# Performance work log

Hardware: AMD Instinct MI355X
Metric: run time of the kernel (lower is better)

The kernel has to match this reference:

```python
import jax, jax.numpy as jnp
import numpy as np

NEG_SLOPE = 0.1

def lrelu(x):
    return jnp.where(x >= 0, x, NEG_SLOPE * x)

def conv1d(x, w, b, stride=2):
    # x: [N, C_in, W], w: [C_out, C_in, K], VALID padding, given stride
    y = jax.lax.conv_general_dilated(x, w, (stride,), 'VALID',
                                     dimension_numbers=('NCH', 'OIH', 'NCH'))
    return y + b[None, :, None]

def setup_inputs() -> dict:
    key = jax.random.key(0)
    ks = jax.random.split(key, 16)
    N_NODES = 50000
    N_EDGES = 4950000
    POS_C, CONV_C, CONV_W = 3, 3, 151
    HID, OUT = 256, 1
    W2 = 37  # width after two stride-2 k=3 convs on 151
    IN_G = POS_C + W2  # 40

    def lin_init(k, fan_out, fan_in):
        s = 1.0 / np.sqrt(fan_in)
        k1, k2 = jax.random.split(k)
        return (jax.random.uniform(k1, (fan_out, fan_in), jnp.float32, -s, s),
                jax.random.uniform(k2, (fan_out,), jnp.float32, -s, s))

    pose = jax.random.normal(ks[0], (N_NODES, POS_C), jnp.float32)
    views = jax.random.normal(ks[1], (N_NODES, CONV_C, CONV_W), jnp.float32)
    edge_index = jax.random.randint(ks[2], (2, N_EDGES), 0, N_NODES, jnp.int64)

    # encoder1: Conv1d(3 -> 9, k=3, s=2); encoder2: Conv1d(9 -> 1, k=3, s=2)
    s1 = 1.0 / np.sqrt(CONV_C * 3)
    w_e1 = jax.random.uniform(ks[3], (CONV_C ** 2, CONV_C, 3), jnp.float32, -s1, s1)
    b_e1 = jax.random.uniform(ks[4], (CONV_C ** 2,), jnp.float32, -s1, s1)
    s2 = 1.0 / np.sqrt(CONV_C ** 2 * 3)
    w_e2 = jax.random.uniform(ks[5], (1, CONV_C ** 2, 3), jnp.float32, -s2, s2)
    b_e2 = jax.random.uniform(ks[6], (1,), jnp.float32, -s2, s2)

    # GraphConv: lin_rel (with bias) on aggregated neighbors, lin_root (no bias) on self
    w_rel, b_rel = lin_init(ks[7], HID, IN_G)
    w_root, _ = lin_init(ks[8], HID, IN_G)

    w_l1, b_l1 = lin_init(ks[9], HID, HID)
    w_l2, b_l2 = lin_init(ks[10], HID, HID)
    w_l3, b_l3 = lin_init(ks[11], HID, HID)
    w_pred, b_pred = lin_init(ks[12], OUT, HID)

    return dict(pose=pose, views=views, edge_index=edge_index,
                w_e1=w_e1, b_e1=b_e1, w_e2=w_e2, b_e2=b_e2,
                w_rel=w_rel, b_rel=b_rel, w_root=w_root,
                w_l1=w_l1, b_l1=b_l1, w_l2=w_l2, b_l2=b_l2,
                w_l3=w_l3, b_l3=b_l3, w_pred=w_pred, b_pred=b_pred)

def reference(pose, views, edge_index, w_e1, b_e1, w_e2, b_e2,
              w_rel, b_rel, w_root,
              w_l1, b_l1, w_l2, b_l2, w_l3, b_l3, w_pred, b_pred):
    n_nodes = pose.shape[0]
    # view encoder
    v = lrelu(conv1d(views, w_e1, b_e1))          # [N, 9, 75]
    v = lrelu(conv1d(v, w_e2, b_e2))              # [N, 1, 37]
    x = jnp.concatenate([pose, v[:, 0, :]], axis=1)  # [N, 40]
    # GraphConv (aggr='add'): out = lin_rel(sum_{j->i} x_j) + lin_root(x_i)
    src, dst = edge_index[0], edge_index[1]
    agg = jax.ops.segment_sum(x[src], dst, num_segments=n_nodes)  # [N, 40]
    h = lrelu(agg @ w_rel.T + b_rel + x @ w_root.T)               # [N, 256]
    # MLP stack (dropout is identity in eval mode)
    h = lrelu(h @ w_l1.T + b_l1)
    h = lrelu(h @ w_l2.T + b_l2)
    h = lrelu(h @ w_l3.T + b_l3)
    return h @ w_pred.T + b_pred  # [N, 1]
```

## Files before the change

### kernel.cpp

```cpp
#include <hip/hip_runtime.h>
#include <hip/hip_fp16.h>

#define NEG_SLOPE 0.1f
__device__ __forceinline__ float lrelu(float v) { return fmaxf(v, NEG_SLOPE * v); }

constexpr int CAP = 8704;
constexpr int EPB = 8192;

typedef __attribute__((ext_vector_type(8))) short short8;
typedef __attribute__((ext_vector_type(4))) float f32x4;

__device__ __forceinline__ unsigned short f2bf(float f) {
    union { float f; unsigned u; } v; v.f = f;
    const unsigned r = v.u + 0x7FFF + ((v.u >> 16) & 1);
    return (unsigned short)(r >> 16);
}
__device__ __forceinline__ float bf2f(unsigned short h) {
    union { unsigned u; float f; } v; v.u = ((unsigned)h) << 16;
    return v.f;
}

__global__ __launch_bounds__(256) void encoder_kernel(
        const float* __restrict__ pose,
        const float* __restrict__ views,
        const float* __restrict__ w1, const float* __restrict__ b1,
        const float* __restrict__ w2, const float* __restrict__ b2,
        const float* __restrict__ w_l1, const float* __restrict__ w_l2,
        const float* __restrict__ w_l3, const float* __restrict__ w_rel,
        const float* __restrict__ w_root,
        unsigned short* __restrict__ Wb1, unsigned short* __restrict__ Wb2,
        unsigned short* __restrict__ Wb3, unsigned short* __restrict__ Wg,
        int* __restrict__ gcur,
        unsigned short* __restrict__ xHi, unsigned short* __restrict__ xLo,
        __half* __restrict__ xh, int N)
{
    __shared__ float s_w1[81];
    __shared__ float s_b1[9];
    __shared__ float s_w2[27];
    __shared__ float s_b2[1];
    __shared__ float s_c1[4][9][80];

    const int t = threadIdx.x;

    if (blockIdx.x < 256) {
        const int i = blockIdx.x * 256 + t;
        Wb1[i] = f2bf(w_l1[i]);
        Wb2[i] = f2bf(w_l2[i]);
        Wb3[i] = f2bf(w_l3[i]);
        if (i < 40960) {
            const int m = i / 160, c = i % 160;
            const int k = c % 80;
            const float v = (k < 40) ? w_rel[m * 40 + k] : w_root[m * 40 + (k - 40)];
            Wg[i] = f2bf(v);
        }
        if (i < 1024) gcur[i] = 0;
        if (i < 40) xh[(size_t)N * 40 + i] = __float2half(0.f);
    }

    if (t < 81) s_w1[t] = w1[t];
    if (t >= 96 && t < 105) s_b1[t - 96] = b1[t - 96];
    if (t >= 128 && t < 155) s_w2[t - 128] = w2[t - 128];
    if (t == 240) s_b2[0] = b2[0];
    __syncthreads();

    const int nb = blockIdx.x * 4;

    #pragma unroll
    for (int pass = 0; pass < 2; pass++) {
        const int task = pass * 256 + t;
        if (task < 300) {
            const int ln = task / 75;
            const int p  = task % 75;
            const int n  = min(nb + ln, N - 1);
            const float* __restrict__ vin = views + (size_t)n * 453 + 2 * p;
            float e[3], o[3], e1[3];
            #pragma unroll
            for (int ic = 0; ic < 3; ic++) {
                const float* ci = vin + ic * 151;
                e[ic] = ci[0]; o[ic] = ci[1]; e1[ic] = ci[2];
            }
            const int didx = (p & 1) * 40 + (p >> 1);
            #pragma unroll
            for (int oc = 0; oc < 9; oc++) {
                float v = s_b1[oc];
                #pragma unroll
                for (int ic = 0; ic < 3; ic++)
                    v += s_w1[oc * 9 + ic * 3 + 0] * e[ic]
                       + s_w1[oc * 9 + ic * 3 + 1] * o[ic]
                       + s_w1[oc * 9 + ic * 3 + 2] * e1[ic];
                s_c1[ln][oc][didx] = lrelu(v);
            }
        }
    }
    __syncthreads();

    if (t < 160) {
        const int ln = t / 40, f = t % 40;
        const int n  = min(nb + ln, N - 1);
        float outv;
        if (f < 3) {
            outv = pose[(size_t)n * 3 + f];
        } else {
            const int ow = f - 3;
            float v = s_b2[0];
            #pragma unroll
            for (int ic = 0; ic < 9; ic++)
                v += s_w2[ic * 3 + 0] * s_c1[ln][ic][ow]
                   + s_w2[ic * 3 + 1] * s_c1[ln][ic][40 + ow]
                   + s_w2[ic * 3 + 2] * s_c1[ln][ic][ow + 1];
            outv = lrelu(v);
        }
        const unsigned short hi = f2bf(outv);
        const unsigned short lo = f2bf(outv - bf2f(hi));
        xHi[(size_t)n * 40 + f] = hi;
        xLo[(size_t)n * 40 + f] = lo;
        xh[(size_t)n * 40 + f] = __float2half(outv);
    }
}

__global__ __launch_bounds__(512) void bin_kernel(
        const int* __restrict__ ei, int* __restrict__ gcur,
        int* __restrict__ pairs, int E, int NB)
{
    __shared__ int s_hist[1024];
    __shared__ int s_loff[1024];
    __shared__ int s_base[1024];
    __shared__ int s_wave8[8];
    __shared__ int s_pk[EPB];
    __shared__ unsigned short s_bkt[EPB];
    const int t = threadIdx.x;
    const int lane = t & 63, wid = t >> 6;
    const int e0 = blockIdx.x * EPB + t * 16;
    const int tot = min(E - (int)blockIdx.x * EPB, EPB);

    for (int i = t; i < 1024; i += 512) s_hist[i] = 0;
    __syncthreads();

    int pk[16], mt[16];
    auto proc = [&](int j, int sv, int dv) {
        const int b = dv >> 6;
        const int r = atomicAdd(&s_hist[b], 1);
        pk[j] = sv * 80 | ((dv & 63) << 22);
        mt[j] = b | (r << 10);
    };

    if (e0 + 16 <= E) {
        #pragma unroll
        for (int q = 0; q < 4; q++) {
            const int4 sv = *(const int4*)(ei + e0 + 4 * q);
            const int4 dv = *(const int4*)(ei + E + e0 + 4 * q);
            proc(4 * q + 0, sv.x, dv.x);
            proc(4 * q + 1, sv.y, dv.y);
            proc(4 * q + 2, sv.z, dv.z);
            proc(4 * q + 3, sv.w, dv.w);
        }
    } else {
        #pragma unroll
        for (int j = 0; j < 16; j++) {
            mt[j] = -1;
            const int e = e0 + j;
            if (e < E) proc(j, ei[e], ei[E + e]);
        }
    }
    __syncthreads();

    int carry = 0;
    #pragma unroll
    for (int base = 0; base < 1024; base += 512) {
        const int i = base + t;
        const int v = s_hist[i];
        int sc = v;
        #pragma unroll
        for (int d = 1; d < 64; d <<= 1) {
            const int u = __shfl_up(sc, d);
            if (lane >= d) sc += u;
        }
        if (lane == 63) s_wave8[wid] = sc;
        __syncthreads();
        if (wid == 0) {
            int wv = (lane < 8) ? s_wave8[lane] : 0;
            #pragma unroll
            for (int d = 1; d < 8; d <<= 1) {
                const int u = __shfl_up(wv, d);
                if (lane >= d) wv += u;
            }
            if (lane < 8) s_wave8[lane] = wv;
        }
        __syncthreads();
        const int waveoff = (wid > 0) ? s_wave8[wid - 1] : 0;
        s_loff[i] = carry + waveoff + sc - v;
        const int chunk_tot = s_wave8[7];
        __syncthreads();
        carry += chunk_tot;
    }

    for (int i = t; i < NB; i += 512) {
        const int c = s_hist[i];
        if (c > 0) s_base[i] = atomicAdd(&gcur[i], c);
    }
    __syncthreads();

    #pragma unroll
    for (int j = 0; j < 16; j++) {
        if (mt[j] >= 0) {
            const int b = mt[j] & 1023;
            const int pos = s_loff[b] + (mt[j] >> 10);
            s_pk[pos] = pk[j];
            s_bkt[pos] = (unsigned short)b;
        }
    }
    __syncthreads();

    for (int i = t; i < tot; i += 512) {
        const int b = s_bkt[i];
        const int p = s_base[b] + (i - s_loff[b]);
        if (p < CAP) pairs[b * CAP + p] = s_pk[i];
    }
}

__global__ __launch_bounds__(512) void sort_gather_kernel(
        const int* __restrict__ gcur,
        const int* __restrict__ pairs,
        const __half* __restrict__ xh,
        unsigned short* __restrict__ aggHi,
        unsigned short* __restrict__ aggLo, int N)
{
    __shared__ int s_sorted[CAP];
    __shared__ int s_cnt[64], s_off[64], s_cur[64];
    const int b = blockIdx.x;
    const int t = threadIdx.x;
    const int cnt = min(gcur[b], CAP);
    const int* __restrict__ pr = pairs + (size_t)b * CAP;

    if (t < 64) s_cnt[t] = 0;
    __syncthreads();
    for (int i = t; i < cnt; i += 512)
        atomicAdd(&s_cnt[pr[i] >> 22], 1);
    __syncthreads();

    if (t < 64) {
        const int c = s_cnt[t];
        const int p = ((c + 23) / 24) * 24;
        int sc = p;
        #pragma unroll
        for (int d = 1; d < 64; d <<= 1) {
            const int u = __shfl_up(sc, d);
            if (t >= d) sc += u;
        }
        const int excl = sc - p;
        s_off[t] = excl;
        s_cur[t] = excl;
    }
    __syncthreads();

    if (t < 64) {
        const int e0 = s_off[t] + s_cnt[t];
        const int e1 = s_off[t] + ((s_cnt[t] + 23) / 24) * 24;
        for (int i = e0; i < e1 && i < CAP; i++) s_sorted[i] = N * 80;
    }
    for (int i = t; i < cnt; i += 512) {
        const int p = pr[i];
        const int pos = atomicAdd(&s_cur[p >> 22], 1);
        if (pos < CAP) s_sorted[pos] = p & 0x3FFFFF;
    }
    __syncthreads();

    const int wave = t >> 6, lane = t & 63;
    const int slot = min(lane / 10, 5);
    const int f4 = lane % 10;
    const char* __restrict__ xb = (const char*)xh + f4 * 8;

    #pragma unroll 1
    for (int i = 0; i < 8; i++) {
        const int ln = wave * 8 + i;
        const int n = b * 64 + ln;
        if (n >= N) break;
        const int c = s_cnt[ln];
        const int cntp = ((c + 23) / 24) * 24;
        const int* __restrict__ srt = s_sorted + s_off[ln] + slot;

        float ax = 0.f, ay = 0.f, az = 0.f, aw = 0.f;
        for (int e = 0; e < cntp; e += 24) {
            const int o0 = srt[e];
            const int o1 = srt[e + 6];
            const int o2 = srt[e + 12];
            const int o3 = srt[e + 18];
            const uint2 u0 = *(const uint2*)(xb + o0);
            const uint2 u1 = *(const uint2*)(xb + o1);
            const uint2 u2 = *(const uint2*)(xb + o2);
            const uint2 u3 = *(const uint2*)(xb + o3);
            union { unsigned u; __half2 h; } cv;
            float2 f;
            cv.u = u0.x; f = __half22float2(cv.h); ax += f.x; ay += f.y;
            cv.u = u0.y; f = __half22float2(cv.h); az += f.x; aw += f.y;
            cv.u = u1.x; f = __half22float2(cv.h); ax += f.x; ay += f.y;
            cv.u = u1.y; f = __half22float2(cv.h); az += f.x; aw += f.y;
            cv.u = u2.x; f = __half22float2(cv.h); ax += f.x; ay += f.y;
            cv.u = u2.y; f = __half22float2(cv.h); az += f.x; aw += f.y;
            cv.u = u3.x; f = __half22float2(cv.h); ax += f.x; ay += f.y;
            cv.u = u3.y; f = __half22float2(cv.h); az += f.x; aw += f.y;
        }

        float rx = ax, ry = ay, rz = az, rw = aw;
        #pragma unroll
        for (int s = 10; s <= 50; s += 10) {
            rx += __shfl(ax, f4 + s);
            ry += __shfl(ay, f4 + s);
            rz += __shfl(az, f4 + s);
            rw += __shfl(aw, f4 + s);
        }
        if (lane < 10) {
            ushort4 hi, lo;
            hi.x = f2bf(rx); lo.x = f2bf(rx - bf2f(hi.x));
            hi.y = f2bf(ry); lo.y = f2bf(ry - bf2f(hi.y));
            hi.z = f2bf(rz); lo.z = f2bf(rz - bf2f(hi.z));
            hi.w = f2bf(rw); lo.w = f2bf(rw - bf2f(hi.w));
            *(ushort4*)(aggHi + (size_t)n * 40 + f4 * 4) = hi;
            *(ushort4*)(aggLo + (size_t)n * 40 + f4 * 4) = lo;
        }
    }
}

__device__ __forceinline__ void gemm_tile(const unsigned short* __restrict__ aT,
                                          const unsigned short* __restrict__ W,
                                          int wstride, int K,
                                          int wave, int l16, int q,
                                          f32x4 acc[4][4])
{
    for (int k0 = 0; k0 < K; k0 += 32) {
        short8 af[4], wf[4];
        #pragma unroll
        for (int nt = 0; nt < 4; nt++)
            af[nt] = *(const short8*)(aT + (nt * 16 + l16) * 264 + k0 + q * 8);
        #pragma unroll
        for (int mt = 0; mt < 4; mt++)
            wf[mt] = *(const short8*)(W + (wave * 64 + mt * 16 + l16) * wstride + k0 + q * 8);
        #pragma unroll
        for (int nt = 0; nt < 4; nt++)
            #pragma unroll
            for (int mt = 0; mt < 4; mt++)
                acc[nt][mt] = __builtin_amdgcn_mfma_f32_16x16x32_bf16(af[nt], wf[mt], acc[nt][mt], 0, 0, 0);
    }
}

__device__ __forceinline__ void epi_to_lds(f32x4 acc[4][4], const float* __restrict__ b,
                                           unsigned short* __restrict__ aT,
                                           int wave, int l16, int q)
{
    float bias[4];
    #pragma unroll
    for (int mt = 0; mt < 4; mt++) bias[mt] = b[wave * 64 + mt * 16 + l16];
    #pragma unroll
    for (int nt = 0; nt < 4; nt++)
        #pragma unroll
        for (int r = 0; r < 4; r++)
            #pragma unroll
            for (int mt = 0; mt < 4; mt++) {
                const int row = nt * 16 + q * 4 + r;
                const int col = wave * 64 + mt * 16 + l16;
                aT[row * 264 + col] = f2bf(lrelu(acc[nt][mt][r] + bias[mt]));
            }
}

__global__ void fused_gemm_kernel(const unsigned short* __restrict__ aggHi,
                                  const unsigned short* __restrict__ aggLo,
                                  const unsigned short* __restrict__ xHi,
                                  const unsigned short* __restrict__ xLo,
                                  const unsigned short* __restrict__ Wg,
                                  const float* __restrict__ b_rel,
                                  const unsigned short* __restrict__ Wb1,
                                  const float* __restrict__ b_l1,
                                  const unsigned short* __restrict__ Wb2,
                                  const float* __restrict__ b_l2,
                                  const unsigned short* __restrict__ Wb3,
                                  const float* __restrict__ b_l3,
                                  const float* __restrict__ w_pred,
                                  const float* __restrict__ b_pred,
                                  float* __restrict__ out, int N)
{
    __shared__ __align__(16) unsigned short aT[64 * 264];
    __shared__ float s_part[4][64];
    const int t = threadIdx.x;
    const int n0 = blockIdx.x * 64;
    const int wave = t >> 6, lane = t & 63, q = lane >> 4, l16 = lane & 15;

    for (int u = t; u < 640; u += 256) {
        const int row = u / 10, c = (u % 10) * 4;
        const int srow = min(n0 + row, N - 1);
        const size_t off = (size_t)srow * 40 + c;
        unsigned short* rp = aT + row * 264;
        *(ushort4*)(rp + c)       = *(const ushort4*)(aggHi + off);
        *(ushort4*)(rp + 40 + c)  = *(const ushort4*)(xHi + off);
        *(ushort4*)(rp + 80 + c)  = *(const ushort4*)(aggLo + off);
        *(ushort4*)(rp + 120 + c) = *(const ushort4*)(xLo + off);
    }
    __syncthreads();

    {
        f32x4 acc[4][4] = {};
        gemm_tile(aT, Wg, 160, 160, wave, l16, q, acc);
        __syncthreads();
        epi_to_lds(acc, b_rel, aT, wave, l16, q);
        __syncthreads();
    }
    {
        f32x4 acc[4][4] = {};
        gemm_tile(aT, Wb1, 256, 256, wave, l16, q, acc);
        __syncthreads();
        epi_to_lds(acc, b_l1, aT, wave, l16, q);
        __syncthreads();
    }
    {
        f32x4 acc[4][4] = {};
        gemm_tile(aT, Wb2, 256, 256, wave, l16, q, acc);
        __syncthreads();
        epi_to_lds(acc, b_l2, aT, wave, l16, q);
        __syncthreads();
    }
    {
        f32x4 acc[4][4] = {};
        gemm_tile(aT, Wb3, 256, 256, wave, l16, q, acc);

        float bias[4], wp[4];
        #pragma unroll
        for (int mt = 0; mt < 4; mt++) {
            const int col = wave * 64 + mt * 16 + l16;
            bias[mt] = b_l3[col];
            wp[mt] = w_pred[col];
        }
        #pragma unroll
        for (int nt = 0; nt < 4; nt++)
            #pragma unroll
            for (int r = 0; r < 4; r++) {
                float p = 0.f;
                #pragma unroll
                for (int mt = 0; mt < 4; mt++)
                    p += lrelu(acc[nt][mt][r] + bias[mt]) * wp[mt];
                p += __shfl_xor(p, 1);
                p += __shfl_xor(p, 2);
                p += __shfl_xor(p, 4);
                p += __shfl_xor(p, 8);
                if (l16 == 0) s_part[wave][nt * 16 + q * 4 + r] = p;
            }
        __syncthreads();

        if (t < 64) {
            const int row = n0 + t;
            if (row < N)
                out[row] = s_part[0][t] + s_part[1][t] + s_part[2][t] + s_part[3][t] + b_pred[0];
        }
    }
}

extern "C" void kernel_launch(void* const* d_in, const int* in_sizes, int n_in,
                              void* d_out, int out_size, void* d_ws, size_t ws_size,
                              hipStream_t stream)
{
    const float* pose   = (const float*)d_in[0];
    const float* views  = (const float*)d_in[1];
    const int*   ei     = (const int*)d_in[2];
    const float* w_e1   = (const float*)d_in[3];
    const float* b_e1   = (const float*)d_in[4];
    const float* w_e2   = (const float*)d_in[5];
    const float* b_e2   = (const float*)d_in[6];
    const float* w_rel  = (const float*)d_in[7];
    const float* b_rel  = (const float*)d_in[8];
    const float* w_root = (const float*)d_in[9];
    const float* w_l1   = (const float*)d_in[10];
    const float* b_l1   = (const float*)d_in[11];
    const float* w_l2   = (const float*)d_in[12];
    const float* b_l2   = (const float*)d_in[13];
    const float* w_l3   = (const float*)d_in[14];
    const float* b_l3   = (const float*)d_in[15];
    const float* w_pred = (const float*)d_in[16];
    const float* b_pred = (const float*)d_in[17];
    float* out = (float*)d_out;

    const int N = in_sizes[0] / 3;
    const int E = in_sizes[2] / 2;
    const int NB = (N + 63) >> 6;
    const int NBLK = (N + 63) / 64;

    unsigned short* xHi = (unsigned short*)d_ws;
    unsigned short* xLo = xHi + (size_t)N * 40;
    unsigned short* aggHi = xLo + (size_t)N * 40;
    unsigned short* aggLo = aggHi + (size_t)N * 40;
    __half* xh = (__half*)(aggLo + (size_t)N * 40);
    int* pairs = (int*)(xh + (size_t)(N + 1) * 40 + 24);
    int* gcur  = pairs + (size_t)NB * CAP;
    unsigned short* Wb1 = (unsigned short*)(gcur + 1024);
    unsigned short* Wb2 = Wb1 + 256 * 256;
    unsigned short* Wb3 = Wb2 + 256 * 256;
    unsigned short* Wg  = Wb3 + 256 * 256;

    encoder_kernel<<<(N + 3) / 4, 256, 0, stream>>>(
        pose, views, w_e1, b_e1, w_e2, b_e2,
        w_l1, w_l2, w_l3, w_rel, w_root,
        Wb1, Wb2, Wb3, Wg, gcur, xHi, xLo, xh, N);

    bin_kernel<<<(E + EPB - 1) / EPB, 512, 0, stream>>>(ei, gcur, pairs, E, NB);

    sort_gather_kernel<<<NB, 512, 0, stream>>>(gcur, pairs, xh, aggHi, aggLo, N);

    fused_gemm_kernel<<<NBLK, 256, 0, stream>>>(
        aggHi, aggLo, xHi, xLo, Wg, b_rel,
        Wb1, b_l1, Wb2, b_l2, Wb3, b_l3,
        w_pred, b_pred, out, N);
}
```

Baseline: 341.3 us.

## Register-cache bucket pairs and widen neighbor gather to 16-byte loads

```diff
diff --git a/kernel.cpp b/kernel.cpp
--- a/kernel.cpp
+++ b/kernel.cpp
@@ -233,9 +233,18 @@
     const int* __restrict__ pr = pairs + (size_t)b * CAP;
 
     if (t < 64) s_cnt[t] = 0;
-    __syncthreads();
-    for (int i = t; i < cnt; i += 512)
-        atomicAdd(&s_cnt[pr[i] >> 22], 1);
+
+    int pk[17];
+    #pragma unroll
+    for (int j = 0; j < 17; j++) {
+        const int i = t + j * 512;
+        pk[j] = (i < cnt) ? __builtin_nontemporal_load(pr + i) : -1;
+    }
+    __syncthreads();
+
+    #pragma unroll
+    for (int j = 0; j < 17; j++)
+        if (pk[j] >= 0) atomicAdd(&s_cnt[pk[j] >> 22], 1);
     __syncthreads();
 
     if (t < 64) {
@@ -258,17 +267,19 @@
         const int e1 = s_off[t] + ((s_cnt[t] + 23) / 24) * 24;
         for (int i = e0; i < e1 && i < CAP; i++) s_sorted[i] = N * 80;
     }
-    for (int i = t; i < cnt; i += 512) {
-        const int p = pr[i];
-        const int pos = atomicAdd(&s_cur[p >> 22], 1);
-        if (pos < CAP) s_sorted[pos] = p & 0x3FFFFF;
+    #pragma unroll
+    for (int j = 0; j < 17; j++) {
+        if (pk[j] >= 0) {
+            const int pos = atomicAdd(&s_cur[pk[j] >> 22], 1);
+            if (pos < CAP) s_sorted[pos] = pk[j] & 0x3FFFFF;
+        }
     }
     __syncthreads();
 
     const int wave = t >> 6, lane = t & 63;
-    const int slot = min(lane / 10, 5);
-    const int f4 = lane % 10;
-    const char* __restrict__ xb = (const char*)xh + f4 * 8;
+    const int slot = min(lane / 5, 11);
+    const int f8 = lane % 5;
+    const char* __restrict__ xb = (const char*)xh + f8 * 16;
 
     #pragma unroll 1
     for (int i = 0; i < 8; i++) {
@@ -279,44 +290,61 @@
         const int cntp = ((c + 23) / 24) * 24;
         const int* __restrict__ srt = s_sorted + s_off[ln] + slot;
 
-        float ax = 0.f, ay = 0.f, az = 0.f, aw = 0.f;
-        for (int e = 0; e < cntp; e += 24) {
+        float a[8];
+        #pragma unroll
+        for (int j = 0; j < 8; j++) a[j] = 0.f;
+
+        union { unsigned v; __half2 h; } cv;
+        float2 f;
+        auto acc8 = [&](uint4 u) {
+            cv.v = u.x; f = __half22float2(cv.h); a[0] += f.x; a[1] += f.y;
+            cv.v = u.y; f = __half22float2(cv.h); a[2] += f.x; a[3] += f.y;
+            cv.v = u.z; f = __half22float2(cv.h); a[4] += f.x; a[5] += f.y;
+            cv.v = u.w; f = __half22float2(cv.h); a[6] += f.x; a[7] += f.y;
+        };
+
+        int e = 0;
+        #pragma unroll 1
+        for (; e + 48 <= cntp; e += 48) {
             const int o0 = srt[e];
-            const int o1 = srt[e + 6];
-            const int o2 = srt[e + 12];
-            const int o3 = srt[e + 18];
-            const uint2 u0 = *(const uint2*)(xb + o0);
-            const uint2 u1 = *(const uint2*)(xb + o1);
-            const uint2 u2 = *(const uint2*)(xb + o2);
-            const uint2 u3 = *(const uint2*)(xb + o3);
-            union { unsigned u; __half2 h; } cv;
-            float2 f;
-            cv.u = u0.x; f = __half22float2(cv.h); ax += f.x; ay += f.y;
-            cv.u = u0.y; f = __half22float2(cv.h); az += f.x; aw += f.y;
-            cv.u = u1.x; f = __half22float2(cv.h); ax += f.x; ay += f.y;
-            cv.u = u1.y; f = __half22float2(cv.h); az += f.x; aw += f.y;
-            cv.u = u2.x; f = __half22float2(cv.h); ax += f.x; ay += f.y;
-            cv.u = u2.y; f = __half22float2(cv.h); az += f.x; aw += f.y;
-            cv.u = u3.x; f = __half22float2(cv.h); ax += f.x; ay += f.y;
-            cv.u = u3.y; f = __half22float2(cv.h); az += f.x; aw += f.y;
-        }
-
-        float rx = ax, ry = ay, rz = az, rw = aw;
-        #pragma unroll
-        for (int s = 10; s <= 50; s += 10) {
-            rx += __shfl(ax, f4 + s);
-            ry += __shfl(ay, f4 + s);
-            rz += __shfl(az, f4 + s);
-            rw += __shfl(aw, f4 + s);
-        }
-        if (lane < 10) {
-            ushort4 hi, lo;
-            hi.x = f2bf(rx); lo.x = f2bf(rx - bf2f(hi.x));
-            hi.y = f2bf(ry); lo.y = f2bf(ry - bf2f(hi.y));
-            hi.z = f2bf(rz); lo.z = f2bf(rz - bf2f(hi.z));
-            hi.w = f2bf(rw); lo.w = f2bf(rw - bf2f(hi.w));
-            *(ushort4*)(aggHi + (size_t)n * 40 + f4 * 4) = hi;
-            *(ushort4*)(aggLo + (size_t)n * 40 + f4 * 4) = lo;
+            const int o1 = srt[e + 12];
+            const int o2 = srt[e + 24];
+            const int o3 = srt[e + 36];
+            const uint4 u0 = *(const uint4*)(xb + o0);
+            const uint4 u1 = *(const uint4*)(xb + o1);
+            const uint4 u2 = *(const uint4*)(xb + o2);
+            const uint4 u3 = *(const uint4*)(xb + o3);
+            acc8(u0); acc8(u1); acc8(u2); acc8(u3);
+        }
+        if (e < cntp) {
+            const int o0 = srt[e];
+            const int o1 = srt[e + 12];
+            const uint4 u0 = *(const uint4*)(xb + o0);
+            const uint4 u1 = *(const uint4*)(xb + o1);
+            acc8(u0); acc8(u1);
+        }
+
+        #pragma unroll
+        for (int j = 0; j < 8; j++) a[j] += __shfl(a[j], lane + 30);
+        #pragma unroll
+        for (int j = 0; j < 8; j++) a[j] += __shfl(a[j], lane + 15);
+        #pragma unroll
+        for (int j = 0; j < 8; j++) a[j] += __shfl(a[j], lane + 5) + __shfl(a[j], lane + 10);
+
+        if (lane < 5) {
+            unsigned short h[8], l[8];
+            #pragma unroll
+            for (int j = 0; j < 8; j++) {
+                h[j] = f2bf(a[j]);
+                l[j] = f2bf(a[j] - bf2f(h[j]));
+            }
+            uint4 H, L;
+            H.x = h[0] | ((unsigned)h[1] << 16); H.y = h[2] | ((unsigned)h[3] << 16);
+            H.z = h[4] | ((unsigned)h[5] << 16); H.w = h[6] | ((unsigned)h[7] << 16);
+            L.x = l[0] | ((unsigned)l[1] << 16); L.y = l[2] | ((unsigned)l[3] << 16);
+            L.z = l[4] | ((unsigned)l[5] << 16); L.w = l[6] | ((unsigned)l[7] << 16);
+            *(uint4*)(aggHi + (size_t)n * 40 + lane * 8) = H;
+            *(uint4*)(aggLo + (size_t)n * 40 + lane * 8) = L;
         }
     }
 }
```

New measurement: 333.9 us. 2.2% less time.
